# Performance work log

Measured on AMD Instinct MI355X. Metric: run time of the kernel, lower is better.

The kernel has to match this reference:

```python
import jax, jax.numpy as jnp
import numpy as np

N_NODES = 100000
N_EDGES = 1600000
IN_CH = 128
HEADS = 4
HEAD_DIM = 16  # out_channels // heads = 64 // 4
EPS = 1e-8
NEG_SLOPE = 0.2


def setup_inputs() -> dict:
    key = jax.random.key(0)
    k1, k2, k3, k4, k5 = jax.random.split(key, 5)
    x = jax.random.normal(k1, (N_NODES, IN_CH), dtype=jnp.float32)
    edge_index = jax.random.randint(k2, (2, N_EDGES), 0, N_NODES, dtype=jnp.int64)
    edge_weight = jax.random.uniform(k3, (N_EDGES,), dtype=jnp.float32)
    # Linear(in_channels, heads*head_dim, bias=False): weight [out, in]
    W = jax.random.normal(k4, (HEADS * HEAD_DIM, IN_CH), dtype=jnp.float32) * 0.05
    a = jax.random.normal(k5, (1, HEADS, 2 * HEAD_DIM), dtype=jnp.float32) * 0.1
    return {"x": x, "edge_index": edge_index, "edge_weight": edge_weight, "W": W, "a": a}


def reference(x, edge_index, edge_weight, W, a):
    num_nodes = x.shape[0]
    h = (x @ W.T).reshape(num_nodes, HEADS, HEAD_DIM)  # [N, H, D]
    src, dst = edge_index[0], edge_index[1]
    h_src = h[src]  # [E, H, D]
    h_dst = h[dst]  # [E, H, D]
    # a * concat(h_src, h_dst) summed over last dim == split-dot (avoids concat)
    a_src = a[..., :HEAD_DIM]  # [1, H, D]
    a_dst = a[..., HEAD_DIM:]  # [1, H, D]
    attention = jnp.sum(a_src * h_src + a_dst * h_dst, axis=-1)  # [E, H]
    attention = jax.nn.leaky_relu(attention, negative_slope=NEG_SLOPE)
    attention = attention * edge_weight[:, None]
    attention = jnp.exp(attention)
    att_sum = jax.ops.segment_sum(attention, dst, num_segments=num_nodes)  # [N, H]
    attention = attention / (att_sum[dst] + EPS)  # [E, H]
    # dropout is identity in eval mode
    weighted = h_src * attention[:, :, None]  # [E, H, D]
    out = jax.ops.segment_sum(weighted, dst, num_segments=num_nodes)  # [N, H, D]
    return out.reshape(num_nodes, HEADS * HEAD_DIM)
```

## Files before the change

kernel.cpp:

```cpp
#include <hip/hip_runtime.h>
#include <math.h>

#define N_NODES 100000
#define N_EDGES 1600000
#define IN_CH 128
#define HEADS 4
#define HEAD_DIM 16
#define OUT_CH 64
#define NEG_SLOPE 0.2f
#define EPS 1e-8f

#define NBUCK 391
#define NBLK1 256
#define CHUNK (N_EDGES / NBLK1)
#define CAPG 4608
#define CAP CAPG

typedef _Float16 f16x8 __attribute__((ext_vector_type(8)));
typedef _Float16 f16x4 __attribute__((ext_vector_type(4)));
typedef float    f32x4 __attribute__((ext_vector_type(4)));

__global__ __launch_bounds__(128) void wsd_kernel(
    const float* __restrict__ W, const float* __restrict__ a,
    float* __restrict__ wsd)
{
    int k = threadIdx.x;
#pragma unroll
    for (int hd = 0; hd < 4; hd++) {
        float ss = 0.f, dd = 0.f;
#pragma unroll
        for (int c = 0; c < 16; c++) {
            float wv = W[(hd * 16 + c) * IN_CH + k];
            ss += a[hd * 32 + c] * wv;
            dd += a[hd * 32 + 16 + c] * wv;
        }
        wsd[hd * IN_CH + k] = ss;
        wsd[(4 + hd) * IN_CH + k] = dd;
    }
}

__device__ inline f16x8 cvt8(const float* p) {
    float4 lo = ((const float4*)p)[0];
    float4 hi = ((const float4*)p)[1];
    f16x8 f;
    f[0] = (_Float16)lo.x; f[1] = (_Float16)lo.y;
    f[2] = (_Float16)lo.z; f[3] = (_Float16)lo.w;
    f[4] = (_Float16)hi.x; f[5] = (_Float16)hi.y;
    f[6] = (_Float16)hi.z; f[7] = (_Float16)hi.w;
    return f;
}

__global__ __launch_bounds__(256) void gemm_alpha_kernel(
    const float* __restrict__ x,
    const float* __restrict__ W,
    const float* __restrict__ wsd,
    _Float16* __restrict__ h,
    float* __restrict__ alpha_src,
    float* __restrict__ alpha_dst)
{
    __shared__ _Float16 hst[128 * 72];

    const int wv = threadIdx.x >> 6;
    const int lane = threadIdx.x & 63;
    const int col = lane & 15;
    const int quad = lane >> 4;
    const int node_base = blockIdx.x * 128 + wv * 32;

    f16x8 bfrag[5][4];
#pragma unroll
    for (int nt = 0; nt < 4; nt++) {
        const float* src = W + (nt * 16 + col) * IN_CH;
#pragma unroll
        for (int ks = 0; ks < 4; ks++)
            bfrag[nt][ks] = cvt8(src + ks * 32 + quad * 8);
    }
    {
        const float* src = wsd + (col < 8 ? col : 0) * IN_CH;
#pragma unroll
        for (int ks = 0; ks < 4; ks++) {
            f16x8 f = cvt8(src + ks * 32 + quad * 8);
            if (col >= 8) {
                f16x8 z = {};
                f = z;
            }
            bfrag[4][ks] = f;
        }
    }

#pragma unroll
    for (int mt = 0; mt < 2; mt++) {
        int row_node = node_base + mt * 16 + col;
        int rn = row_node < N_NODES ? row_node : N_NODES - 1;
        const float* xrow = x + (long long)rn * IN_CH;

        f16x8 afrag[4];
#pragma unroll
        for (int ks = 0; ks < 4; ks++)
            afrag[ks] = cvt8(xrow + ks * 32 + quad * 8);

        f32x4 acc[5];
#pragma unroll
        for (int nt = 0; nt < 5; nt++) {
            f32x4 z = {0.f, 0.f, 0.f, 0.f};
            acc[nt] = z;
        }
#pragma unroll
        for (int ks = 0; ks < 4; ks++)
#pragma unroll
            for (int nt = 0; nt < 5; nt++)
                acc[nt] = __builtin_amdgcn_mfma_f32_16x16x32_f16(
                    afrag[ks], bfrag[nt][ks], acc[nt], 0, 0, 0);

#pragma unroll
        for (int r = 0; r < 4; r++) {
            int nl = wv * 32 + mt * 16 + quad * 4 + r;
#pragma unroll
            for (int nt = 0; nt < 4; nt++)
                hst[nl * 72 + nt * 16 + col] = (_Float16)acc[nt][r];
            int node = node_base + mt * 16 + quad * 4 + r;
            if (node < N_NODES) {
                if (col < 4)      alpha_src[node * HEADS + col]     = acc[4][r];
                else if (col < 8) alpha_dst[node * HEADS + col - 4] = acc[4][r];
            }
        }
    }

    __syncthreads();
    const int bnode = blockIdx.x * 128;
    const int nrem = N_NODES - bnode;
    const int climit = (nrem < 128 ? nrem : 128) << 3;
    for (int i = threadIdx.x; i < 1024; i += 256) {
        if (i < climit) {
            int node = i >> 3, ch8 = i & 7;
            *(f16x8*)(h + (long long)(bnode + node) * OUT_CH + ch8 * 8) =
                *(const f16x8*)&hst[node * 72 + ch8 * 8];
        }
    }
}

__global__ __launch_bounds__(256) void fused_count_scatter_kernel(
    const int* __restrict__ ei, const float* __restrict__ ew,
    int* __restrict__ gcur,
    unsigned long long* __restrict__ tmp)
{
    __shared__ int cnt[NBUCK];
    __shared__ int dbuf[CHUNK];
    for (int j = threadIdx.x; j < NBUCK; j += 256) cnt[j] = 0;
    __syncthreads();
    const int base = blockIdx.x * CHUNK;
    for (int i = threadIdx.x; i < CHUNK; i += 256) {
        int d = ei[N_EDGES + base + i];
        dbuf[i] = d;
        atomicAdd(&cnt[d >> 8], 1);
    }
    __syncthreads();
    for (int j = threadIdx.x; j < NBUCK; j += 256) {
        int c = cnt[j];
        int b = (c > 0) ? atomicAdd(&gcur[j], c) : 0;
        cnt[j] = j * CAPG + b;
    }
    __syncthreads();
    for (int i = threadIdx.x; i < CHUNK; i += 256) {
        int e = base + i;
        int d = dbuf[i];
        int s = ei[e];
        float w = ew[e];
        int pos = atomicAdd(&cnt[d >> 8], 1);
        unsigned long long pk = ((unsigned long long)__float_as_uint(w) << 32)
                              | ((unsigned)(d & 255) << 17) | (unsigned)s;
        tmp[pos] = pk;
    }
}

__global__ __launch_bounds__(512) void bucket_offsets_kernel(
    const int* __restrict__ gcur, int* __restrict__ bucketStart,
    int* __restrict__ ptr)
{
    __shared__ int part[512];
    const int t = threadIdx.x;
    int v = (t < NBUCK) ? gcur[t] : 0;
    part[t] = v;
    __syncthreads();
    for (int off = 1; off < 512; off <<= 1) {
        int x = (t >= off) ? part[t - off] : 0;
        __syncthreads();
        part[t] += x;
        __syncthreads();
    }
    if (t < NBUCK) bucketStart[t] = part[t] - v;
    if (t == 0) { bucketStart[NBUCK] = N_EDGES; ptr[N_NODES] = N_EDGES; }
}

__global__ __launch_bounds__(256) void finalize_kernel(
    const unsigned long long* __restrict__ tmp,
    const int* __restrict__ gcur,
    const int* __restrict__ bucketStart,
    long long* __restrict__ csr, int* __restrict__ ptr)
{
    __shared__ int cnt[256];
    __shared__ int offs[256];
    __shared__ unsigned long long stage[CAP];
    const int j = blockIdx.x;
    const int t = threadIdx.x;
    const int beg = bucketStart[j];
    const int len = gcur[j];
    const unsigned long long* src = tmp + (size_t)j * CAPG;

    cnt[t] = 0;
    __syncthreads();

    for (int i = t; i < len; i += 256) {
        unsigned long long pk = __builtin_nontemporal_load(&src[i]);
        stage[i] = pk;
        atomicAdd(&cnt[(int)((pk >> 17) & 255)], 1);
    }
    __syncthreads();
    int v = cnt[t];
    for (int off = 1; off < 256; off <<= 1) {
        int x = (t >= off) ? cnt[t - off] : 0;
        __syncthreads();
        cnt[t] += x;
        __syncthreads();
    }
    int excl = cnt[t] - v;
    int node = j * 256 + t;
    if (node < N_NODES) ptr[node] = beg + excl;
    offs[t] = excl;
    __syncthreads();
    for (int i = t; i < len; i += 256) {
        unsigned long long pk = stage[i];
        int dloc = (int)((pk >> 17) & 255);
        int pos = atomicAdd(&offs[dloc], 1);
        unsigned long long vv = (pk & 0xFFFFFFFF00000000ull) | (pk & 0x1FFFFull);
        ((unsigned long long*)csr)[beg + pos] = vv;
    }
}

__global__ __launch_bounds__(256) void aggregate_kernel(
    const int* __restrict__ ptr,
    const int2* __restrict__ csr,
    const float4* __restrict__ alpha_src4,
    const float4* __restrict__ alpha_dst4,
    const _Float16* __restrict__ h,
    float* __restrict__ out)
{
    __shared__ float4 sev[4][64];
    __shared__ int    ssc[4][64];

    const int wv = threadIdx.x >> 6;
    const int lane = threadIdx.x & 63;
    const int n = blockIdx.x * 4 + wv;
    if (n >= N_NODES) return;
    const int q = lane >> 4;
    const int cg = lane & 15;
    const int hsel = cg >> 2;

    const int beg = ptr[n];
    const int end = ptr[n + 1];
    const float4 ad4 = alpha_dst4[n];

    float4 acc = make_float4(0.f, 0.f, 0.f, 0.f);
    float denom = 0.f;
    float4* sev_w = sev[wv];
    int* ssc_w = ssc[wv];

    for (int base = beg; base < end; base += 64) {
        int cnt = min(64, end - base);
        int s_l = 0;
        float4 e4 = make_float4(0.f, 0.f, 0.f, 0.f);
        if (lane < cnt) {
            int2 pr = csr[base + lane];
            s_l = pr.x;
            float w = __int_as_float(pr.y);
            float4 as = alpha_src4[s_l];
            float t0 = as.x + ad4.x; t0 = (t0 > 0.f ? t0 : NEG_SLOPE * t0) * w;
            float t1 = as.y + ad4.y; t1 = (t1 > 0.f ? t1 : NEG_SLOPE * t1) * w;
            float t2 = as.z + ad4.z; t2 = (t2 > 0.f ? t2 : NEG_SLOPE * t2) * w;
            float t3 = as.w + ad4.w; t3 = (t3 > 0.f ? t3 : NEG_SLOPE * t3) * w;
            e4 = make_float4(__expf(t0), __expf(t1), __expf(t2), __expf(t3));
        }
        sev_w[lane] = e4;
        ssc_w[lane] = s_l;

        int iters = (cnt + 3) >> 2;
        for (int j0 = 0; j0 < iters; j0 += 2) {
            int idx0 = j0 * 4 + q;
            int idx1 = idx0 + 4;
            int s0 = ssc_w[idx0];
            int s1 = ssc_w[idx1];
            float ev0 = ((const float*)&sev_w[idx0])[hsel];
            float ev1 = ((const float*)&sev_w[idx1])[hsel];
            f16x4 h0 = *(const f16x4*)(h + s0 * OUT_CH + cg * 4);
            f16x4 h1 = *(const f16x4*)(h + s1 * OUT_CH + cg * 4);
            acc.x += ev0 * (float)h0[0] + ev1 * (float)h1[0];
            acc.y += ev0 * (float)h0[1] + ev1 * (float)h1[1];
            acc.z += ev0 * (float)h0[2] + ev1 * (float)h1[2];
            acc.w += ev0 * (float)h0[3] + ev1 * (float)h1[3];
            denom += ev0 + ev1;
        }
    }

    denom += __shfl_xor(denom, 16);
    denom += __shfl_xor(denom, 32);
    acc.x += __shfl_xor(acc.x, 16);  acc.x += __shfl_xor(acc.x, 32);
    acc.y += __shfl_xor(acc.y, 16);  acc.y += __shfl_xor(acc.y, 32);
    acc.z += __shfl_xor(acc.z, 16);  acc.z += __shfl_xor(acc.z, 32);
    acc.w += __shfl_xor(acc.w, 16);  acc.w += __shfl_xor(acc.w, 32);

    if (lane < 16) {
        float inv = 1.f / (denom + EPS);
        float4 r = make_float4(acc.x * inv, acc.y * inv, acc.z * inv, acc.w * inv);
        ((float4*)(out + (long long)n * OUT_CH))[cg] = r;
    }
}

extern "C" void kernel_launch(void* const* d_in, const int* in_sizes, int n_in,
                              void* d_out, int out_size, void* d_ws, size_t ws_size,
                              hipStream_t stream) {
    const float* x  = (const float*)d_in[0];
    const int*   ei = (const int*)d_in[1];
    const float* ew = (const float*)d_in[2];
    const float* W  = (const float*)d_in[3];
    const float* a  = (const float*)d_in[4];
    float* out = (float*)d_out;

    char* p = (char*)d_ws;
    _Float16* h      = (_Float16*)p; p += (size_t)N_NODES * OUT_CH * 2;
    float* alpha_src = (float*)p;  p += (size_t)N_NODES * HEADS * 4;
    float* alpha_dst = (float*)p;  p += (size_t)N_NODES * HEADS * 4;
    float* wsd       = (float*)p;  p += (size_t)8 * IN_CH * 4;
    int*   gcur      = (int*)p;    p += (size_t)392 * 4;
    int*   bstart    = (int*)p;    p += (size_t)392 * 4;
    int*   ptr       = (int*)p;    p += (size_t)(N_NODES + 4) * 4;
    unsigned long long* tmp = (unsigned long long*)p;
    p += (size_t)NBUCK * CAPG * 8;
    long long* csr   = (long long*)p;

    hipMemsetAsync(gcur, 0, 392 * sizeof(int), stream);

    wsd_kernel<<<1, 128, 0, stream>>>(W, a, wsd);
    fused_count_scatter_kernel<<<NBLK1, 256, 0, stream>>>(ei, ew, gcur, tmp);
    bucket_offsets_kernel<<<1, 512, 0, stream>>>(gcur, bstart, ptr);
    gemm_alpha_kernel<<<(N_NODES + 127) / 128, 256, 0, stream>>>(x, W, wsd, h, alpha_src, alpha_dst);
    finalize_kernel<<<NBUCK, 256, 0, stream>>>(tmp, gcur, bstart, csr, ptr);
    aggregate_kernel<<<(N_NODES + 3) / 4, 256, 0, stream>>>(
        ptr, (const int2*)csr, (const float4*)alpha_src, (const float4*)alpha_dst, h, out);
}
```

Baseline: 215.2 us.

## Pre-convert weights to fp16, reuse first-pass ranks in finalize, double scatter blocks

After: 211.0 us. Within noise of the previous version (-1.9%).

```diff
diff --git a/kernel.cpp b/kernel.cpp
--- a/kernel.cpp
+++ b/kernel.cpp
@@ -11,7 +11,7 @@
 #define EPS 1e-8f
 
 #define NBUCK 391
-#define NBLK1 256
+#define NBLK1 512
 #define CHUNK (N_EDGES / NBLK1)
 #define CAPG 4608
 #define CAP CAPG
@@ -20,11 +20,14 @@
 typedef _Float16 f16x4 __attribute__((ext_vector_type(4)));
 typedef float    f32x4 __attribute__((ext_vector_type(4)));
 
-__global__ __launch_bounds__(128) void wsd_kernel(
+__global__ __launch_bounds__(128) void prep16_kernel(
     const float* __restrict__ W, const float* __restrict__ a,
-    float* __restrict__ wsd)
+    _Float16* __restrict__ Wh)
 {
     int k = threadIdx.x;
+#pragma unroll
+    for (int r = 0; r < 64; r++)
+        Wh[r * IN_CH + k] = (_Float16)W[r * IN_CH + k];
 #pragma unroll
     for (int hd = 0; hd < 4; hd++) {
         float ss = 0.f, dd = 0.f;
@@ -34,8 +37,8 @@
             ss += a[hd * 32 + c] * wv;
             dd += a[hd * 32 + 16 + c] * wv;
         }
-        wsd[hd * IN_CH + k] = ss;
-        wsd[(4 + hd) * IN_CH + k] = dd;
+        Wh[(64 + hd) * IN_CH + k] = (_Float16)ss;
+        Wh[(68 + hd) * IN_CH + k] = (_Float16)dd;
     }
 }
 
@@ -52,8 +55,7 @@
 
 __global__ __launch_bounds__(256) void gemm_alpha_kernel(
     const float* __restrict__ x,
-    const float* __restrict__ W,
-    const float* __restrict__ wsd,
+    const _Float16* __restrict__ Wh,
     _Float16* __restrict__ h,
     float* __restrict__ alpha_src,
     float* __restrict__ alpha_dst)
@@ -69,16 +71,16 @@
     f16x8 bfrag[5][4];
 #pragma unroll
     for (int nt = 0; nt < 4; nt++) {
-        const float* src = W + (nt * 16 + col) * IN_CH;
+        const _Float16* src = Wh + (nt * 16 + col) * IN_CH;
 #pragma unroll
         for (int ks = 0; ks < 4; ks++)
-            bfrag[nt][ks] = cvt8(src + ks * 32 + quad * 8);
+            bfrag[nt][ks] = *(const f16x8*)(src + ks * 32 + quad * 8);
     }
     {
-        const float* src = wsd + (col < 8 ? col : 0) * IN_CH;
+        const _Float16* src = Wh + (64 + (col < 8 ? col : 0)) * IN_CH;
 #pragma unroll
         for (int ks = 0; ks < 4; ks++) {
-            f16x8 f = cvt8(src + ks * 32 + quad * 8);
+            f16x8 f = *(const f16x8*)(src + ks * 32 + quad * 8);
             if (col >= 8) {
                 f16x8 z = {};
                 f = z;
@@ -199,6 +201,7 @@
 {
     __shared__ int cnt[256];
     __shared__ int offs[256];
+    __shared__ unsigned short rk[CAP];
     __shared__ unsigned long long stage[CAP];
     const int j = blockIdx.x;
     const int t = threadIdx.x;
@@ -212,7 +215,7 @@
     for (int i = t; i < len; i += 256) {
         unsigned long long pk = __builtin_nontemporal_load(&src[i]);
         stage[i] = pk;
-        atomicAdd(&cnt[(int)((pk >> 17) & 255)], 1);
+        rk[i] = (unsigned short)atomicAdd(&cnt[(int)((pk >> 17) & 255)], 1);
     }
     __syncthreads();
     int v = cnt[t];
@@ -230,7 +233,7 @@
     for (int i = t; i < len; i += 256) {
         unsigned long long pk = stage[i];
         int dloc = (int)((pk >> 17) & 255);
-        int pos = atomicAdd(&offs[dloc], 1);
+        int pos = offs[dloc] + (int)rk[i];
         unsigned long long vv = (pk & 0xFFFFFFFF00000000ull) | (pk & 0x1FFFFull);
         ((unsigned long long*)csr)[beg + pos] = vv;
     }
@@ -328,7 +331,7 @@
     _Float16* h      = (_Float16*)p; p += (size_t)N_NODES * OUT_CH * 2;
     float* alpha_src = (float*)p;  p += (size_t)N_NODES * HEADS * 4;
     float* alpha_dst = (float*)p;  p += (size_t)N_NODES * HEADS * 4;
-    float* wsd       = (float*)p;  p += (size_t)8 * IN_CH * 4;
+    _Float16* Wh     = (_Float16*)p; p += (size_t)72 * IN_CH * 2;
     int*   gcur      = (int*)p;    p += (size_t)392 * 4;
     int*   bstart    = (int*)p;    p += (size_t)392 * 4;
     int*   ptr       = (int*)p;    p += (size_t)(N_NODES + 4) * 4;
@@ -338,10 +341,10 @@
 
     hipMemsetAsync(gcur, 0, 392 * sizeof(int), stream);
 
-    wsd_kernel<<<1, 128, 0, stream>>>(W, a, wsd);
+    prep16_kernel<<<1, 128, 0, stream>>>(W, a, Wh);
     fused_count_scatter_kernel<<<NBLK1, 256, 0, stream>>>(ei, ew, gcur, tmp);
     bucket_offsets_kernel<<<1, 512, 0, stream>>>(gcur, bstart, ptr);
-    gemm_alpha_kernel<<<(N_NODES + 127) / 128, 256, 0, stream>>>(x, W, wsd, h, alpha_src, alpha_dst);
+    gemm_alpha_kernel<<<(N_NODES + 127) / 128, 256, 0, stream>>>(x, Wh, h, alpha_src, alpha_dst);
     finalize_kernel<<<NBUCK, 256, 0, stream>>>(tmp, gcur, bstart, csr, ptr);
     aggregate_kernel<<<(N_NODES + 3) / 4, 256, 0, stream>>>(
         ptr, (const int2*)csr, (const float4*)alpha_src, (const float4*)alpha_dst, h, out);
```
